# Optimization experiments

Measured on AMD Instinct MI355X. Metric: run time of the kernel, lower is better.

Reference implementation:

```python
import jax, jax.numpy as jnp
import numpy as np

DIM = 1024
HEADS = 16
HEAD_DIM = 64
ROT_DIM = HEAD_DIM // 2  # RotaryEmbedding(dim=head_dim//2): rotates first 32 dims only
B, T, H, W = 2, 32, 18, 32


def setup_inputs() -> dict:
    key = jax.random.key(0)
    k1, k2, k3 = jax.random.split(key, 3)
    x = jax.random.normal(k1, (B, T, H, W, DIM), dtype=jnp.float32)
    w_qkv = jax.random.normal(k2, (3 * HEADS * HEAD_DIM, DIM), dtype=jnp.float32) * 0.02
    w_out = jax.random.normal(k3, (DIM, HEADS * HEAD_DIM), dtype=jnp.float32) * 0.02
    b_out = jnp.zeros((DIM,), dtype=jnp.float32)
    return {"x": x, "w_qkv": w_qkv, "w_out": w_out, "b_out": b_out}


def _rope(t, pos):
    # t: [N, h, T, d]. lucidrains convention: interleaved pairs, rotate first ROT_DIM dims.
    freqs = 1.0 / (10000.0 ** (jnp.arange(0, ROT_DIM, 2, dtype=jnp.float32) / ROT_DIM))  # [ROT_DIM/2]
    ang = pos[:, None] * freqs[None, :]          # [T, ROT_DIM/2]
    ang = jnp.repeat(ang, 2, axis=-1)            # [T, ROT_DIM] (each freq repeated for its pair)
    cos, sin = jnp.cos(ang), jnp.sin(ang)
    x_rot, x_pass = t[..., :ROT_DIM], t[..., ROT_DIM:]
    xr = x_rot.reshape(x_rot.shape[:-1] + (ROT_DIM // 2, 2))
    rot = jnp.stack([-xr[..., 1], xr[..., 0]], axis=-1).reshape(x_rot.shape)  # rotate_half
    return jnp.concatenate([x_rot * cos + rot * sin, x_pass], axis=-1)


def reference(x, w_qkv, w_out, b_out):
    b, t, h, w, d = x.shape
    # fused QKV projection (bias=False)
    qkv = jnp.einsum('bthwd,ed->bthwe', x, w_qkv)
    q, k, v = jnp.split(qkv, 3, axis=-1)

    def to_heads(u):
        # 'B T H W (h d) -> (B H W) h T d'
        u = u.reshape(b, t, h, w, HEADS, HEAD_DIM)
        return u.transpose(0, 2, 3, 4, 1, 5).reshape(b * h * w, HEADS, t, HEAD_DIM)

    q, k, v = to_heads(q), to_heads(k), to_heads(v)
    pos = jnp.arange(t, dtype=jnp.float32)
    q = _rope(q, pos)
    k = _rope(k, pos)

    scale = HEAD_DIM ** -0.5
    scores = jnp.einsum('nhqd,nhkd->nhqk', q, k) * scale  # [BHW, h, T, T]
    causal = jnp.tril(jnp.ones((t, t), dtype=bool))
    scores = jnp.where(causal, scores, -jnp.inf)
    attn = jax.nn.softmax(scores, axis=-1)
    o = jnp.einsum('nhqk,nhkd->nhqd', attn, v)
    # '(B H W) h T d -> B T H W (h d)'
    o = o.reshape(b, h, w, HEADS, t, HEAD_DIM).transpose(0, 4, 1, 2, 3, 5)
    o = o.reshape(b, t, h, w, HEADS * HEAD_DIM)
    return o @ w_out.T + b_out
```

## Files before the change

kernel.cpp:

```cpp
#include <hip/hip_runtime.h>
#include <cstdint>
#include <cstddef>

typedef __bf16 bf16;
typedef __attribute__((ext_vector_type(8))) bf16  bf16x8;
typedef __attribute__((ext_vector_type(4))) bf16  bf16x4;
typedef __attribute__((ext_vector_type(4))) float f32x4;

#define B_SZ   2
#define T_SZ   32
#define H_SZ   18
#define W_SZ   32
#define DIM    1024
#define NHEAD  16
#define HDIM   64
#define E3     3072
#define M_TOT  36864
#define T_STRIDE 576
#define GK     1024
#define NKT    16

__global__ void taa_cvt_bf16(const float* __restrict__ s, bf16* __restrict__ d, int n4) {
    int i = blockIdx.x * 256 + threadIdx.x;
    if (i >= n4) return;
    float4 v = ((const float4*)s)[i];
    bf16x4 o;
    o.x = (bf16)v.x; o.y = (bf16)v.y; o.z = (bf16)v.z; o.w = (bf16)v.w;
    ((bf16x4*)d)[i] = o;
}

__device__ __forceinline__ void async_copy_16(const bf16* g, bf16* l) {
    __builtin_amdgcn_global_load_lds((__attribute__((address_space(1))) void*)g,
                                     (__attribute__((address_space(3))) void*)l,
                                     16, 0, 0);
}

#define MFMA16(a, b, c) __builtin_amdgcn_mfma_f32_16x16x32_bf16((a), (b), (c), 0, 0, 0)

template<bool OUT_BF16>
__global__ __launch_bounds__(512, 2)
void taa_gemm256(const bf16* __restrict__ A, const bf16* __restrict__ Bm,
                 void* __restrict__ Cout, const float* __restrict__ bias, int N) {
    __shared__ __align__(16) bf16 sA[2][2][8192];
    __shared__ __align__(16) bf16 sB[2][2][8192];

    const int tid  = threadIdx.x;
    const int lane = tid & 63;
    const int wv   = tid >> 6;
    const int wm   = wv >> 2;
    const int wn   = wv & 3;
    const int fr   = lane & 15;
    const int fq   = lane >> 4;

    const int ntn = N >> 8;
    const int nwg = gridDim.x;
    const int bid = blockIdx.x;
    const int swz = (bid & 7) * (nwg >> 3) + (bid >> 3);
    const int bm  = (swz / ntn) << 8;
    const int bn  = (swz % ntn) << 8;

    const int srow = tid >> 3;
    const int scol = ((tid & 7) ^ (srow & 7)) << 3;
    const bf16* gA0 = A  + (size_t)(bm + srow) * GK + scol;
    const bf16* gB0 = Bm + (size_t)(bn + srow) * GK + scol;

    const int swx = (fr & 7) << 4;
    const int cs0 = (fq * 16) ^ swx;
    const int cs1 = (64 + fq * 16) ^ swx;

    f32x4 acc[2][2][4][2];
#pragma unroll
    for (int ms = 0; ms < 2; ms++)
#pragma unroll
        for (int ns = 0; ns < 2; ns++)
#pragma unroll
            for (int i = 0; i < 4; i++)
#pragma unroll
                for (int j = 0; j < 2; j++)
                    acc[ms][ns][i][j] = (f32x4){0.f, 0.f, 0.f, 0.f};

    auto stage = [&](const bf16* g0, bf16* lbase, int h, int kt) {
        const bf16* g = g0 + (size_t)(h * 128) * GK + kt * 64;
        async_copy_16(g,                    lbase + h * 8192 + tid * 8);
        async_copy_16(g + (size_t)64 * GK,  lbase + h * 8192 + 4096 + tid * 8);
    };

    stage(gB0, &sB[0][0][0], 0, 0); stage(gB0, &sB[0][0][0], 1, 0);
    stage(gA0, &sA[0][0][0], 0, 0); stage(gA0, &sA[0][0][0], 1, 0);
    stage(gB0, &sB[1][0][0], 0, 1); stage(gB0, &sB[1][0][0], 1, 1);
    stage(gA0, &sA[1][0][0], 0, 1); stage(gA0, &sA[1][0][0], 1, 1);
    asm volatile("s_waitcnt vmcnt(8)" ::: "memory");
    __builtin_amdgcn_s_barrier();
    asm volatile("" ::: "memory");

    bf16x8 af[4][2];
    bf16x8 bfr[2][2][2];

#pragma unroll 2
    for (int kt = 0; kt < NKT; ++kt) {
        const int buf = kt & 1;
        const char* ab = (const char*)&sA[buf][wm][0] + fr * 128;
        const char* bb = (const char*)&sB[buf][wn >> 1][0] + ((wn & 1) * 64 + fr) * 128;
        const bool st = (kt + 2 < NKT);

#pragma unroll
        for (int i = 0; i < 4; i++) {
            af[i][0] = *(const bf16x8*)(ab + i * 2048 + cs0);
            af[i][1] = *(const bf16x8*)(ab + i * 2048 + cs1);
        }
#pragma unroll
        for (int j = 0; j < 2; j++) {
            bfr[0][j][0] = *(const bf16x8*)(bb + j * 2048 + cs0);
            bfr[0][j][1] = *(const bf16x8*)(bb + j * 2048 + cs1);
        }
        asm volatile("" ::: "memory");
        __builtin_amdgcn_s_barrier();
        asm volatile("s_waitcnt lgkmcnt(0)" ::: "memory");
        __builtin_amdgcn_sched_barrier(0);
        __builtin_amdgcn_s_setprio(1);
#pragma unroll
        for (int i = 0; i < 4; i++)
#pragma unroll
            for (int j = 0; j < 2; j++) {
                acc[0][0][i][j] = MFMA16(af[i][0], bfr[0][j][0], acc[0][0][i][j]);
                acc[0][0][i][j] = MFMA16(af[i][1], bfr[0][j][1], acc[0][0][i][j]);
            }
        __builtin_amdgcn_s_setprio(0);
        asm volatile("" ::: "memory");
        __builtin_amdgcn_s_barrier();
        asm volatile("" ::: "memory");

#pragma unroll
        for (int j = 0; j < 2; j++) {
            bfr[1][j][0] = *(const bf16x8*)(bb + 4096 + j * 2048 + cs0);
            bfr[1][j][1] = *(const bf16x8*)(bb + 4096 + j * 2048 + cs1);
        }
        asm volatile("" ::: "memory");
        __builtin_amdgcn_s_barrier();
        asm volatile("s_waitcnt lgkmcnt(0)" ::: "memory");
        __builtin_amdgcn_sched_barrier(0);
        __builtin_amdgcn_s_setprio(1);
#pragma unroll
        for (int i = 0; i < 4; i++)
#pragma unroll
            for (int j = 0; j < 2; j++) {
                acc[0][1][i][j] = MFMA16(af[i][0], bfr[1][j][0], acc[0][1][i][j]);
                acc[0][1][i][j] = MFMA16(af[i][1], bfr[1][j][1], acc[0][1][i][j]);
            }
        __builtin_amdgcn_s_setprio(0);
        asm volatile("" ::: "memory");
        __builtin_amdgcn_s_barrier();
        asm volatile("" ::: "memory");

#pragma unroll
        for (int i = 0; i < 4; i++) {
            af[i][0] = *(const bf16x8*)(ab + 8192 + i * 2048 + cs0);
            af[i][1] = *(const bf16x8*)(ab + 8192 + i * 2048 + cs1);
        }
        if (st) {
            stage(gB0, &sB[buf][0][0], 0, kt + 2);
            stage(gB0, &sB[buf][0][0], 1, kt + 2);
        }
        asm volatile("" ::: "memory");
        __builtin_amdgcn_s_barrier();
        asm volatile("s_waitcnt lgkmcnt(0)" ::: "memory");
        __builtin_amdgcn_sched_barrier(0);
        __builtin_amdgcn_s_setprio(1);
#pragma unroll
        for (int i = 0; i < 4; i++)
#pragma unroll
            for (int j = 0; j < 2; j++) {
                acc[1][1][i][j] = MFMA16(af[i][0], bfr[1][j][0], acc[1][1][i][j]);
                acc[1][1][i][j] = MFMA16(af[i][1], bfr[1][j][1], acc[1][1][i][j]);
            }
        __builtin_amdgcn_s_setprio(0);
        asm volatile("" ::: "memory");
        __builtin_amdgcn_s_barrier();
        asm volatile("" ::: "memory");

        if (st) {
            stage(gA0, &sA[buf][0][0], 0, kt + 2);
            stage(gA0, &sA[buf][0][0], 1, kt + 2);
        }
        asm volatile("" ::: "memory");
        __builtin_amdgcn_s_barrier();
        __builtin_amdgcn_sched_barrier(0);
        __builtin_amdgcn_s_setprio(1);
#pragma unroll
        for (int i = 0; i < 4; i++)
#pragma unroll
            for (int j = 0; j < 2; j++) {
                acc[1][0][i][j] = MFMA16(af[i][0], bfr[0][j][0], acc[1][0][i][j]);
                acc[1][0][i][j] = MFMA16(af[i][1], bfr[0][j][1], acc[1][0][i][j]);
            }
        __builtin_amdgcn_s_setprio(0);
        if (kt < NKT - 2) asm volatile("s_waitcnt vmcnt(8)" ::: "memory");
        else              asm volatile("s_waitcnt vmcnt(0)" ::: "memory");
        asm volatile("" ::: "memory");
        __builtin_amdgcn_s_barrier();
        asm volatile("" ::: "memory");
    }

    if constexpr (OUT_BF16) {
        bf16* C = (bf16*)Cout;
#pragma unroll
        for (int ms = 0; ms < 2; ms++)
#pragma unroll
            for (int ns = 0; ns < 2; ns++)
#pragma unroll
                for (int i = 0; i < 4; i++)
#pragma unroll
                    for (int j = 0; j < 2; j++)
#pragma unroll
                        for (int r = 0; r < 4; r++) {
                            const int row = bm + wm * 128 + ms * 64 + i * 16 + fq * 4 + r;
                            const int col = bn + wn * 64 + ns * 32 + j * 16 + fr;
                            C[(size_t)row * N + col] = (bf16)acc[ms][ns][i][j][r];
                        }
    } else {
        float* C = (float*)Cout;
#pragma unroll
        for (int ms = 0; ms < 2; ms++)
#pragma unroll
            for (int ns = 0; ns < 2; ns++)
#pragma unroll
                for (int i = 0; i < 4; i++)
#pragma unroll
                    for (int j = 0; j < 2; j++)
#pragma unroll
                        for (int r = 0; r < 4; r++) {
                            const int row = bm + wm * 128 + ms * 64 + i * 16 + fq * 4 + r;
                            const int col = bn + wn * 64 + ns * 32 + j * 16 + fr;
                            C[(size_t)row * N + col] = acc[ms][ns][i][j][r] + bias[col];
                        }
    }
}

__global__ __launch_bounds__(64)
void taa_attn_mfma(const bf16* __restrict__ qkv, bf16* __restrict__ o) {
    __shared__ __align__(16) bf16 sQ[32 * 72];
    __shared__ __align__(16) bf16 sK[32 * 72];
    __shared__ __align__(16) bf16 sVt[64 * 40];
    __shared__ __align__(16) bf16 sP[32 * 40];

    const int lane = threadIdx.x;
    const int bid  = blockIdx.x;
    const int head = bid & 15;
    const int n    = bid >> 4;
    const int w_sp = n & 31;
    const int h_sp = (n >> 5) % 18;
    const int b    = n / (18 * 32);
    const int m0   = b * 18432 + h_sp * 32 + w_sp;

    {
        const int tl = lane >> 3;
        const int dl = (lane & 7) * 8;
#pragma unroll
        for (int it = 0; it < 4; ++it) {
            const int t = it * 8 + tl;
            const size_t rb = (size_t)(m0 + t * T_STRIDE) * E3 + head * 64 + dl;
            bf16x8 q8 = *(const bf16x8*)(qkv + rb);
            bf16x8 k8 = *(const bf16x8*)(qkv + rb + 1024);
            bf16x8 v8 = *(const bf16x8*)(qkv + rb + 2048);
            float qf[8], kf[8];
#pragma unroll
            for (int j = 0; j < 8; j++) { qf[j] = (float)q8[j]; kf[j] = (float)k8[j]; }
            if (dl < 32) {
#pragma unroll
                for (int p = 0; p < 4; p++) {
                    const int fi = dl / 2 + p;
                    float freq = exp2f(-(float)fi * 0.830482024f);
                    float ang  = (float)t * freq;
                    float s, c;
                    sincosf(ang, &s, &c);
                    float a = qf[2 * p], bb = qf[2 * p + 1];
                    qf[2 * p]     = a * c - bb * s;
                    qf[2 * p + 1] = bb * c + a * s;
                    a = kf[2 * p]; bb = kf[2 * p + 1];
                    kf[2 * p]     = a * c - bb * s;
                    kf[2 * p + 1] = bb * c + a * s;
                }
            }
            bf16x8 qo, ko;
#pragma unroll
            for (int j = 0; j < 8; j++) { qo[j] = (bf16)qf[j]; ko[j] = (bf16)kf[j]; }
            *(bf16x8*)&sQ[t * 72 + dl] = qo;
            *(bf16x8*)&sK[t * 72 + dl] = ko;
#pragma unroll
            for (int j = 0; j < 8; j++) sVt[(dl + j) * 40 + t] = v8[j];
        }
    }
    __syncthreads();

    const int fr = lane & 15;
    const int fq = lane >> 4;

    f32x4 S[2][2];
#pragma unroll
    for (int mt = 0; mt < 2; mt++)
#pragma unroll
        for (int nt = 0; nt < 2; nt++) S[mt][nt] = (f32x4){0.f, 0.f, 0.f, 0.f};

    bf16x8 kb0[2], kb1[2];
#pragma unroll
    for (int nt = 0; nt < 2; nt++) {
        kb0[nt] = *(const bf16x8*)&sK[(nt * 16 + fr) * 72 + fq * 8];
        kb1[nt] = *(const bf16x8*)&sK[(nt * 16 + fr) * 72 + 32 + fq * 8];
    }
#pragma unroll
    for (int mt = 0; mt < 2; mt++) {
        bf16x8 a0 = *(const bf16x8*)&sQ[(mt * 16 + fr) * 72 + fq * 8];
        bf16x8 a1 = *(const bf16x8*)&sQ[(mt * 16 + fr) * 72 + 32 + fq * 8];
#pragma unroll
        for (int nt = 0; nt < 2; nt++) {
            S[mt][nt] = __builtin_amdgcn_mfma_f32_16x16x32_bf16(a0, kb0[nt], S[mt][nt], 0, 0, 0);
            S[mt][nt] = __builtin_amdgcn_mfma_f32_16x16x32_bf16(a1, kb1[nt], S[mt][nt], 0, 0, 0);
        }
    }

    float P[2][2][4];
#pragma unroll
    for (int mt = 0; mt < 2; mt++) {
#pragma unroll
        for (int r = 0; r < 4; r++) {
            const int row = mt * 16 + fq * 4 + r;
            float s0 = S[mt][0][r] * 0.125f;
            float s1 = S[mt][1][r] * 0.125f;
            if (fr > row)      s0 = -1e30f;
            if (16 + fr > row) s1 = -1e30f;
            float mx = fmaxf(s0, s1);
#pragma unroll
            for (int mk = 1; mk <= 8; mk <<= 1) mx = fmaxf(mx, __shfl_xor(mx, mk, 64));
            float e0 = __expf(s0 - mx);
            float e1 = __expf(s1 - mx);
            float sm = e0 + e1;
#pragma unroll
            for (int mk = 1; mk <= 8; mk <<= 1) sm += __shfl_xor(sm, mk, 64);
            float inv = 1.0f / sm;
            P[mt][0][r] = e0 * inv;
            P[mt][1][r] = e1 * inv;
        }
    }

#pragma unroll
    for (int mt = 0; mt < 2; mt++)
#pragma unroll
        for (int nt = 0; nt < 2; nt++)
#pragma unroll
            for (int r = 0; r < 4; r++)
                sP[(mt * 16 + fq * 4 + r) * 40 + nt * 16 + fr] = (bf16)P[mt][nt][r];
    __syncthreads();

    f32x4 O[2][4];
#pragma unroll
    for (int mt = 0; mt < 2; mt++)
#pragma unroll
        for (int dt = 0; dt < 4; dt++) O[mt][dt] = (f32x4){0.f, 0.f, 0.f, 0.f};
#pragma unroll
    for (int mt = 0; mt < 2; mt++) {
        bf16x8 a = *(const bf16x8*)&sP[(mt * 16 + fr) * 40 + fq * 8];
#pragma unroll
        for (int dt = 0; dt < 4; dt++) {
            bf16x8 bv = *(const bf16x8*)&sVt[(dt * 16 + fr) * 40 + fq * 8];
            O[mt][dt] = __builtin_amdgcn_mfma_f32_16x16x32_bf16(a, bv, O[mt][dt], 0, 0, 0);
        }
    }

#pragma unroll
    for (int mt = 0; mt < 2; mt++)
#pragma unroll
        for (int dt = 0; dt < 4; dt++)
#pragma unroll
            for (int r = 0; r < 4; r++) {
                const int t = mt * 16 + fq * 4 + r;
                const int d = dt * 16 + fr;
                o[(size_t)(m0 + t * T_STRIDE) * DIM + head * 64 + d] = (bf16)O[mt][dt][r];
            }
}

extern "C" void kernel_launch(void* const* d_in, const int* in_sizes, int n_in,
                              void* d_out, int out_size, void* d_ws, size_t ws_size,
                              hipStream_t stream) {
    const float* x     = (const float*)d_in[0];
    const float* w_qkv = (const float*)d_in[1];
    const float* w_out = (const float*)d_in[2];
    const float* b_out = (const float*)d_in[3];

    char* ws = (char*)d_ws;
    bf16* x_b    = (bf16*)(ws + 0);
    bf16* wqkv_b = (bf16*)(ws + 75497472);
    bf16* wout_b = (bf16*)(ws + 81788928);
    bf16* qkv_b  = (bf16*)(ws + 83886080);
    bf16* o_b    = (bf16*)(ws + 310378496);

    taa_cvt_bf16<<<(M_TOT * DIM / 4 + 255) / 256, 256, 0, stream>>>(x, x_b, M_TOT * DIM / 4);
    taa_cvt_bf16<<<(E3 * DIM / 4 + 255) / 256, 256, 0, stream>>>(w_qkv, wqkv_b, E3 * DIM / 4);
    taa_cvt_bf16<<<(DIM * DIM / 4 + 255) / 256, 256, 0, stream>>>(w_out, wout_b, DIM * DIM / 4);

    taa_gemm256<true><<<dim3((M_TOT / 256) * (E3 / 256)), 512, 0, stream>>>(
        x_b, wqkv_b, (void*)qkv_b, nullptr, E3);

    taa_attn_mfma<<<1152 * 16, 64, 0, stream>>>(qkv_b, o_b);

    taa_gemm256<false><<<dim3((M_TOT / 256) * (DIM / 256)), 512, 0, stream>>>(
        o_b, wout_b, d_out, b_out, DIM);
}
```

Before: 719.2 us.

## Load all LDS fragments up front and cut GEMM barriers; use fast sincos

The GEMM main loop used to run four ping-pong phases, each with its own barrier and lgkmcnt wait. It now issues every LDS fragment read for the K-tile at the start (A for both halves, B for both halves) and runs the MFMAs in two groups, so only two barriers remain per iteration. This removes barrier and wait overhead and gives the compiler room to overlap LDS reads with MFMAs, but it keeps more VGPRs live, which may lower occupancy or cause spills. Separately, the RoPE step now uses the fast __sincosf intrinsic instead of precise sincosf, which is less accurate for larger angles.

```diff
diff --git a/kernel.cpp b/kernel.cpp
--- a/kernel.cpp
+++ b/kernel.cpp
@@ -93,9 +93,6 @@
     __builtin_amdgcn_s_barrier();
     asm volatile("" ::: "memory");
 
-    bf16x8 af[4][2];
-    bf16x8 bfr[2][2][2];
-
 #pragma unroll 2
     for (int kt = 0; kt < NKT; ++kt) {
         const int buf = kt & 1;
@@ -103,100 +100,79 @@
         const char* bb = (const char*)&sB[buf][wn >> 1][0] + ((wn & 1) * 64 + fr) * 128;
         const bool st = (kt + 2 < NKT);
 
-#pragma unroll
-        for (int i = 0; i < 4; i++) {
+        bf16x8 af[4][2];
+        bf16x8 ag[4][2];
+        bf16x8 bf0[2][2];
+        bf16x8 bf1[2][2];
+
+        af[0][0] = *(const bf16x8*)(ab + cs0);
+        af[0][1] = *(const bf16x8*)(ab + cs1);
+#pragma unroll
+        for (int j = 0; j < 2; j++) {
+            bf0[j][0] = *(const bf16x8*)(bb + j * 2048 + cs0);
+            bf0[j][1] = *(const bf16x8*)(bb + j * 2048 + cs1);
+        }
+#pragma unroll
+        for (int i = 1; i < 4; i++) {
             af[i][0] = *(const bf16x8*)(ab + i * 2048 + cs0);
             af[i][1] = *(const bf16x8*)(ab + i * 2048 + cs1);
         }
 #pragma unroll
         for (int j = 0; j < 2; j++) {
-            bfr[0][j][0] = *(const bf16x8*)(bb + j * 2048 + cs0);
-            bfr[0][j][1] = *(const bf16x8*)(bb + j * 2048 + cs1);
-        }
-        asm volatile("" ::: "memory");
-        __builtin_amdgcn_s_barrier();
+            bf1[j][0] = *(const bf16x8*)(bb + 4096 + j * 2048 + cs0);
+            bf1[j][1] = *(const bf16x8*)(bb + 4096 + j * 2048 + cs1);
+        }
+#pragma unroll
+        for (int i = 0; i < 4; i++) {
+            ag[i][0] = *(const bf16x8*)(ab + 8192 + i * 2048 + cs0);
+            ag[i][1] = *(const bf16x8*)(ab + 8192 + i * 2048 + cs1);
+        }
+
+        __builtin_amdgcn_s_setprio(1);
+#pragma unroll
+        for (int i = 0; i < 4; i++)
+#pragma unroll
+            for (int j = 0; j < 2; j++) {
+                acc[0][0][i][j] = MFMA16(af[i][0], bf0[j][0], acc[0][0][i][j]);
+                acc[0][0][i][j] = MFMA16(af[i][1], bf0[j][1], acc[0][0][i][j]);
+            }
+#pragma unroll
+        for (int i = 0; i < 4; i++)
+#pragma unroll
+            for (int j = 0; j < 2; j++) {
+                acc[0][1][i][j] = MFMA16(af[i][0], bf1[j][0], acc[0][1][i][j]);
+                acc[0][1][i][j] = MFMA16(af[i][1], bf1[j][1], acc[0][1][i][j]);
+            }
+        __builtin_amdgcn_s_setprio(0);
+
         asm volatile("s_waitcnt lgkmcnt(0)" ::: "memory");
-        __builtin_amdgcn_sched_barrier(0);
-        __builtin_amdgcn_s_setprio(1);
-#pragma unroll
-        for (int i = 0; i < 4; i++)
-#pragma unroll
-            for (int j = 0; j < 2; j++) {
-                acc[0][0][i][j] = MFMA16(af[i][0], bfr[0][j][0], acc[0][0][i][j]);
-                acc[0][0][i][j] = MFMA16(af[i][1], bfr[0][j][1], acc[0][0][i][j]);
-            }
-        __builtin_amdgcn_s_setprio(0);
-        asm volatile("" ::: "memory");
         __builtin_amdgcn_s_barrier();
         asm volatile("" ::: "memory");
 
-#pragma unroll
-        for (int j = 0; j < 2; j++) {
-            bfr[1][j][0] = *(const bf16x8*)(bb + 4096 + j * 2048 + cs0);
-            bfr[1][j][1] = *(const bf16x8*)(bb + 4096 + j * 2048 + cs1);
-        }
-        asm volatile("" ::: "memory");
-        __builtin_amdgcn_s_barrier();
-        asm volatile("s_waitcnt lgkmcnt(0)" ::: "memory");
-        __builtin_amdgcn_sched_barrier(0);
-        __builtin_amdgcn_s_setprio(1);
-#pragma unroll
-        for (int i = 0; i < 4; i++)
-#pragma unroll
-            for (int j = 0; j < 2; j++) {
-                acc[0][1][i][j] = MFMA16(af[i][0], bfr[1][j][0], acc[0][1][i][j]);
-                acc[0][1][i][j] = MFMA16(af[i][1], bfr[1][j][1], acc[0][1][i][j]);
-            }
-        __builtin_amdgcn_s_setprio(0);
-        asm volatile("" ::: "memory");
-        __builtin_amdgcn_s_barrier();
-        asm volatile("" ::: "memory");
-
-#pragma unroll
-        for (int i = 0; i < 4; i++) {
-            af[i][0] = *(const bf16x8*)(ab + 8192 + i * 2048 + cs0);
-            af[i][1] = *(const bf16x8*)(ab + 8192 + i * 2048 + cs1);
-        }
         if (st) {
             stage(gB0, &sB[buf][0][0], 0, kt + 2);
             stage(gB0, &sB[buf][0][0], 1, kt + 2);
-        }
-        asm volatile("" ::: "memory");
-        __builtin_amdgcn_s_barrier();
-        asm volatile("s_waitcnt lgkmcnt(0)" ::: "memory");
-        __builtin_amdgcn_sched_barrier(0);
-        __builtin_amdgcn_s_setprio(1);
-#pragma unroll
-        for (int i = 0; i < 4; i++)
-#pragma unroll
-            for (int j = 0; j < 2; j++) {
-                acc[1][1][i][j] = MFMA16(af[i][0], bfr[1][j][0], acc[1][1][i][j]);
-                acc[1][1][i][j] = MFMA16(af[i][1], bfr[1][j][1], acc[1][1][i][j]);
-            }
-        __builtin_amdgcn_s_setprio(0);
-        asm volatile("" ::: "memory");
-        __builtin_amdgcn_s_barrier();
-        asm volatile("" ::: "memory");
-
-        if (st) {
             stage(gA0, &sA[buf][0][0], 0, kt + 2);
             stage(gA0, &sA[buf][0][0], 1, kt + 2);
         }
-        asm volatile("" ::: "memory");
-        __builtin_amdgcn_s_barrier();
-        __builtin_amdgcn_sched_barrier(0);
         __builtin_amdgcn_s_setprio(1);
 #pragma unroll
         for (int i = 0; i < 4; i++)
 #pragma unroll
             for (int j = 0; j < 2; j++) {
-                acc[1][0][i][j] = MFMA16(af[i][0], bfr[0][j][0], acc[1][0][i][j]);
-                acc[1][0][i][j] = MFMA16(af[i][1], bfr[0][j][1], acc[1][0][i][j]);
+                acc[1][1][i][j] = MFMA16(ag[i][0], bf1[j][0], acc[1][1][i][j]);
+                acc[1][1][i][j] = MFMA16(ag[i][1], bf1[j][1], acc[1][1][i][j]);
+            }
+#pragma unroll
+        for (int i = 0; i < 4; i++)
+#pragma unroll
+            for (int j = 0; j < 2; j++) {
+                acc[1][0][i][j] = MFMA16(ag[i][0], bf0[j][0], acc[1][0][i][j]);
+                acc[1][0][i][j] = MFMA16(ag[i][1], bf0[j][1], acc[1][0][i][j]);
             }
         __builtin_amdgcn_s_setprio(0);
         if (kt < NKT - 2) asm volatile("s_waitcnt vmcnt(8)" ::: "memory");
         else              asm volatile("s_waitcnt vmcnt(0)" ::: "memory");
-        asm volatile("" ::: "memory");
         __builtin_amdgcn_s_barrier();
         asm volatile("" ::: "memory");
     }
@@ -272,7 +248,7 @@
                     float freq = exp2f(-(float)fi * 0.830482024f);
                     float ang  = (float)t * freq;
                     float s, c;
-                    sincosf(ang, &s, &c);
+                    __sincosf(ang, &s, &c);
                     float a = qf[2 * p], bb = qf[2 * p + 1];
                     qf[2 * p]     = a * c - bb * s;
                     qf[2 * p + 1] = bb * c + a * s;
```

Result: faster. 695.7 us (-3.3%).
